# Kernel tuning notes

Measured on AMD Instinct MI355X. Metric: run time of the kernel, lower is better.

The kernel has to match this reference:

```python
import jax, jax.numpy as jnp
import numpy as np

N = 8192
F_IN = 256
F_OUT = 256


def setup_inputs() -> dict:
    key = jax.random.key(0)
    k1, k2, k3 = jax.random.split(key, 3)
    H = jax.random.normal(k1, (N, F_IN), dtype=jnp.float32)
    A_tilde = jax.random.uniform(k2, (N, N), dtype=jnp.float32)  # positive -> valid degrees
    # xavier_uniform for W: limit = sqrt(6/(fan_in+fan_out))
    limit = np.sqrt(6.0 / (F_IN + F_OUT)).astype(np.float32)
    W = jax.random.uniform(k3, (F_IN, F_OUT), dtype=jnp.float32, minval=-limit, maxval=limit)
    return {"H": H, "A_tilde": A_tilde, "W": W}


def reference(H, A_tilde, W):
    # H(l+1) = relu(D^-1/2 A D^-1/2 H W)
    # Diagonal matmuls expressed as row/col rescaling (same math, O(N^2)).
    d_inv_sqrt = jnp.sum(A_tilde, axis=1) ** -0.5          # [N]
    A_norm = d_inv_sqrt[:, None] * A_tilde * d_inv_sqrt[None, :]  # [N,N]
    H_next = (A_norm @ H) @ W                              # [N,F_out]
    return jax.nn.relu(H_next)
```

## Files before the change

### kernel.cpp

```cpp
#include <hip/hip_runtime.h>
#include <hip/hip_bf16.h>

#define N_ROWS 8192
#define F_DIM  256

typedef __bf16 bf16x8_t __attribute__((ext_vector_type(8)));
typedef float  f32x4_t  __attribute__((ext_vector_type(4)));
typedef float  f32x2_t  __attribute__((ext_vector_type(2)));

static __device__ __forceinline__ unsigned short f2bf(float x) {
    union { __hip_bfloat16 h; unsigned short u; } c;
    c.h = __float2bfloat16(x);
    return c.u;
}
static __device__ __forceinline__ unsigned pk2(float lo, float hi) {
    return (unsigned)f2bf(lo) | ((unsigned)f2bf(hi) << 16);
}

__global__ __launch_bounds__(256) void wconv_kernel(const float* __restrict__ W,
                                                    unsigned short* __restrict__ Ws) {
    const int kb = blockIdx.x;
    const int t  = threadIdx.x;
    __shared__ float wt[32][257];
    const int r = t >> 3, g = t & 7;
    const float* src = W + (kb * 32 + r) * F_DIM + g * 32;
#pragma unroll
    for (int i = 0; i < 8; ++i) {
        float4 v = *(const float4*)(src + i * 4);
        wt[r][g * 32 + i * 4 + 0] = v.x;
        wt[r][g * 32 + i * 4 + 1] = v.y;
        wt[r][g * 32 + i * 4 + 2] = v.z;
        wt[r][g * 32 + i * 4 + 3] = v.w;
    }
    __syncthreads();
    unsigned o[16];
#pragma unroll
    for (int k = 0; k < 32; k += 2) o[k >> 1] = pk2(wt[k][t], wt[k + 1][t]);
    uint4* dst = (uint4*)(Ws + kb * 8192 + t * 32);
#pragma unroll
    for (int i = 0; i < 4; ++i) dst[i] = make_uint4(o[4*i], o[4*i+1], o[4*i+2], o[4*i+3]);
}

__global__ __launch_bounds__(256) void pass1_kernel(const float* __restrict__ A,
                                                    float* __restrict__ rowsum,
                                                    unsigned short* __restrict__ As) {
    const int r    = (int)((blockIdx.x * 256 + threadIdx.x) >> 6);
    const int lane = threadIdx.x & 63;
    const float* src = A + ((size_t)r << 13) + lane * 8;
    const int m = r & 15, mt = (r >> 4) & 1;
    unsigned short* tbase = As + (size_t)(r >> 5) * (128 * 2048) + mt * 128 + m * 8;

    f32x4_t acc0 = {0.f, 0.f, 0.f, 0.f}, acc1 = {0.f, 0.f, 0.f, 0.f};
#pragma unroll 4
    for (int it = 0; it < 16; ++it) {
        const int c0 = it * 512 + lane * 8;
        f32x4_t v0 = __builtin_nontemporal_load((f32x4_t*)(src + it * 512));
        f32x4_t v1 = __builtin_nontemporal_load((f32x4_t*)(src + it * 512 + 4));
        acc0 += v0; acc1 += v1;
        uint4 pkd;
        pkd.x = pk2(v0[0], v0[1]); pkd.y = pk2(v0[2], v0[3]);
        pkd.z = pk2(v1[0], v1[1]); pkd.w = pk2(v1[2], v1[3]);
        const size_t soff = (size_t)(c0 >> 6) * 2048
                          + (size_t)((c0 >> 5) & 1) * 1024
                          + (size_t)((c0 >> 3) & 3) * 256;
        *(uint4*)(tbase + soff) = pkd;
    }
    f32x4_t a = acc0 + acc1;
    float s = (a[0] + a[1]) + (a[2] + a[3]);
#pragma unroll
    for (int off = 1; off < 64; off <<= 1) s += __shfl_xor(s, off);
    if (lane == 0) rowsum[r] = s;
}

__global__ __launch_bounds__(256) void prep2_kernel(const float* __restrict__ rowsum,
                                                    const float* __restrict__ H,
                                                    float* __restrict__ dvec,
                                                    unsigned short* __restrict__ Xs) {
    const int kb = blockIdx.x;
    const int t  = threadIdx.x;
    __shared__ float dl[32];
    __shared__ float ht[32][257];
    if (t < 32) {
        float d = 1.0f / sqrtf(rowsum[kb * 32 + t]);
        dl[t] = d;
        dvec[kb * 32 + t] = d;
    }
    __syncthreads();
    const int hr = t >> 3, hg = t & 7;
    const float* hsrc = H + (size_t)(kb * 32 + hr) * F_DIM + hg * 32;
    const float d = dl[hr];
#pragma unroll
    for (int i = 0; i < 8; ++i) {
        float4 v = *(const float4*)(hsrc + i * 4);
        ht[hr][hg * 32 + i * 4 + 0] = v.x * d;
        ht[hr][hg * 32 + i * 4 + 1] = v.y * d;
        ht[hr][hg * 32 + i * 4 + 2] = v.z * d;
        ht[hr][hg * 32 + i * 4 + 3] = v.w * d;
    }
    __syncthreads();
    unsigned o[16];
#pragma unroll
    for (int k = 0; k < 32; k += 2) o[k >> 1] = pk2(ht[k][t], ht[k + 1][t]);
    uint4* dst = (uint4*)(Xs + kb * 8192 + t * 32);
#pragma unroll
    for (int i = 0; i < 4; ++i) dst[i] = make_uint4(o[4*i], o[4*i+1], o[4*i+2], o[4*i+3]);
}

template <int KITERS>
__global__ __launch_bounds__(512) void gemm1_kernel(const unsigned short* __restrict__ As,
                                                    const unsigned short* __restrict__ Bs,
                                                    const float* __restrict__ dvec,
                                                    float* __restrict__ Y) {
    const int t    = threadIdx.x;
    const int blk  = blockIdx.x;
    const int half = blockIdx.y;
    const int w = t >> 6, l = t & 63;
    const int m = l & 15, q = l >> 4;

    const unsigned short* ap = As + ((size_t)blk * 128 + (size_t)half * KITERS) * 2048
                                  + q * 256 + m * 8;
    const unsigned short* bp = Bs + (size_t)half * KITERS * 16384 + (w * 32 + m) * 32 + q * 8;

    f32x4_t acc[2][2] = {};

    uint4 a_cur[4], b_cur[4];
    a_cur[0] = *(const uint4*)(ap);
    a_cur[1] = *(const uint4*)(ap + 128);
    a_cur[2] = *(const uint4*)(ap + 1024);
    a_cur[3] = *(const uint4*)(ap + 1152);
    b_cur[0] = *(const uint4*)(bp);
    b_cur[1] = *(const uint4*)(bp + 512);
    b_cur[2] = *(const uint4*)(bp + 8192);
    b_cur[3] = *(const uint4*)(bp + 8704);

    for (int i = 0; i < KITERS; ++i) {
        uint4 a_nxt[4], b_nxt[4];
        if (i + 1 < KITERS) {
            const unsigned short* an = ap + (size_t)(i + 1) * 2048;
            const unsigned short* bn = bp + (size_t)(i + 1) * 16384;
            a_nxt[0] = *(const uint4*)(an);
            a_nxt[1] = *(const uint4*)(an + 128);
            a_nxt[2] = *(const uint4*)(an + 1024);
            a_nxt[3] = *(const uint4*)(an + 1152);
            b_nxt[0] = *(const uint4*)(bn);
            b_nxt[1] = *(const uint4*)(bn + 512);
            b_nxt[2] = *(const uint4*)(bn + 8192);
            b_nxt[3] = *(const uint4*)(bn + 8704);
        }
#pragma unroll
        for (int s = 0; s < 2; ++s) {
            bf16x8_t af0 = __builtin_bit_cast(bf16x8_t, a_cur[s * 2 + 0]);
            bf16x8_t af1 = __builtin_bit_cast(bf16x8_t, a_cur[s * 2 + 1]);
            bf16x8_t bf0 = __builtin_bit_cast(bf16x8_t, b_cur[s * 2 + 0]);
            bf16x8_t bf1 = __builtin_bit_cast(bf16x8_t, b_cur[s * 2 + 1]);
            acc[0][0] = __builtin_amdgcn_mfma_f32_16x16x32_bf16(af0, bf0, acc[0][0], 0, 0, 0);
            acc[0][1] = __builtin_amdgcn_mfma_f32_16x16x32_bf16(af0, bf1, acc[0][1], 0, 0, 0);
            acc[1][0] = __builtin_amdgcn_mfma_f32_16x16x32_bf16(af1, bf0, acc[1][0], 0, 0, 0);
            acc[1][1] = __builtin_amdgcn_mfma_f32_16x16x32_bf16(af1, bf1, acc[1][1], 0, 0, 0);
        }
#pragma unroll
        for (int k = 0; k < 4; ++k) { a_cur[k] = a_nxt[k]; b_cur[k] = b_nxt[k]; }
    }

    float* obase = Y + (size_t)half * ((size_t)N_ROWS * F_DIM);
    const int gcol0 = w * 32 + m;
#pragma unroll
    for (int mt = 0; mt < 2; ++mt) {
#pragma unroll
        for (int r = 0; r < 4; ++r) {
            const int grow = blk * 32 + mt * 16 + q * 4 + r;
            const float ds = dvec[grow];
#pragma unroll
            for (int nt = 0; nt < 2; ++nt) {
                obase[(size_t)grow * F_DIM + gcol0 + nt * 16] = acc[mt][nt][r] * ds;
            }
        }
    }
}

template <int KITERS, int ASTRIDE>
__global__ __launch_bounds__(512) void gemm2_kernel(const float* __restrict__ Amat,
                                                    const float* __restrict__ Amat2,
                                                    const unsigned short* __restrict__ Bs,
                                                    float* __restrict__ out) {
    const int t   = threadIdx.x;
    const int blk = blockIdx.x;
    const int w = t >> 6, l = t & 63;
    const int m = l & 15, q = l >> 4;

    __shared__ __align__(16) unsigned short Al[2][1024];

    const int ar = t >> 4, ac = (t & 15) * 2;
    const float* aptr  = Amat  + (size_t)(blk * 32 + ar) * ASTRIDE + ac;
    const float* aptr2 = Amat2 + (size_t)(blk * 32 + ar) * ASTRIDE + ac;
    const int wr_idx = (ac >> 3) * 256 + (ar >> 4) * 128 + (ar & 15) * 8 + (ac & 7);

    const unsigned short* bptr = Bs + (w * 32 + m) * 32 + q * 8;

    f32x4_t acc[2][2] = {};

    f32x2_t a_cur[2]; uint4 b_cur[2][2];
#pragma unroll
    for (int s = 0; s < 2; ++s) {
        f32x2_t a1 = *(const f32x2_t*)(aptr + s * 32);
        f32x2_t a2 = *(const f32x2_t*)(aptr2 + s * 32);
        a_cur[s] = a1 + a2;
        b_cur[s][0] = *(const uint4*)(bptr + s * 8192);
        b_cur[s][1] = *(const uint4*)(bptr + s * 8192 + 512);
    }

    for (int i = 0; i < KITERS; ++i) {
        f32x2_t a_nxt[2]; uint4 b_nxt[2][2];
        if (i + 1 < KITERS) {
            const float* ap  = aptr  + (i + 1) * 64;
            const float* ap2 = aptr2 + (i + 1) * 64;
            const unsigned short* bp = bptr + (size_t)(i + 1) * 16384;
#pragma unroll
            for (int s = 0; s < 2; ++s) {
                f32x2_t a1 = *(const f32x2_t*)(ap + s * 32);
                f32x2_t a2 = *(const f32x2_t*)(ap2 + s * 32);
                a_nxt[s] = a1 + a2;
                b_nxt[s][0] = *(const uint4*)(bp + s * 8192);
                b_nxt[s][1] = *(const uint4*)(bp + s * 8192 + 512);
            }
        }
        const unsigned aw0 = pk2(a_cur[0][0], a_cur[0][1]);
        const unsigned aw1 = pk2(a_cur[1][0], a_cur[1][1]);
        __syncthreads();
        *(unsigned*)&Al[0][wr_idx] = aw0;
        *(unsigned*)&Al[1][wr_idx] = aw1;
        __syncthreads();
#pragma unroll
        for (int s = 0; s < 2; ++s) {
            bf16x8_t af0 = *(const bf16x8_t*)&Al[s][q * 256 + m * 8];
            bf16x8_t af1 = *(const bf16x8_t*)&Al[s][q * 256 + 128 + m * 8];
            bf16x8_t bf0 = __builtin_bit_cast(bf16x8_t, b_cur[s][0]);
            bf16x8_t bf1 = __builtin_bit_cast(bf16x8_t, b_cur[s][1]);
            acc[0][0] = __builtin_amdgcn_mfma_f32_16x16x32_bf16(af0, bf0, acc[0][0], 0, 0, 0);
            acc[0][1] = __builtin_amdgcn_mfma_f32_16x16x32_bf16(af0, bf1, acc[0][1], 0, 0, 0);
            acc[1][0] = __builtin_amdgcn_mfma_f32_16x16x32_bf16(af1, bf0, acc[1][0], 0, 0, 0);
            acc[1][1] = __builtin_amdgcn_mfma_f32_16x16x32_bf16(af1, bf1, acc[1][1], 0, 0, 0);
        }
#pragma unroll
        for (int s = 0; s < 2; ++s) {
            a_cur[s]    = a_nxt[s];
            b_cur[s][0] = b_nxt[s][0];
            b_cur[s][1] = b_nxt[s][1];
        }
    }

    const int gcol0 = w * 32 + m;
#pragma unroll
    for (int mt = 0; mt < 2; ++mt) {
#pragma unroll
        for (int r = 0; r < 4; ++r) {
            const int grow = blk * 32 + mt * 16 + q * 4 + r;
#pragma unroll
            for (int nt = 0; nt < 2; ++nt) {
                out[(size_t)grow * F_DIM + gcol0 + nt * 16] = fmaxf(acc[mt][nt][r], 0.f);
            }
        }
    }
}

extern "C" void kernel_launch(void* const* d_in, const int* in_sizes, int n_in,
                              void* d_out, int out_size, void* d_ws, size_t ws_size,
                              hipStream_t stream) {
    (void)in_sizes; (void)n_in; (void)out_size; (void)ws_size;
    const float* H = (const float*)d_in[0];
    const float* A = (const float*)d_in[1];
    const float* W = (const float*)d_in[2];
    float* out = (float*)d_out;

    char* ws = (char*)d_ws;
    float*          dvec   = (float*)ws;
    float*          rowsum = (float*)(ws + (32 << 10));
    unsigned short* Wsz    = (unsigned short*)(ws + (64 << 10));
    unsigned short* Xs     = (unsigned short*)(ws + (256 << 10));
    float*          Y1     = (float*)(ws + (8 << 20));
    float*          Y2     = Y1 + (size_t)N_ROWS * F_DIM;
    unsigned short* As     = (unsigned short*)(ws + (32 << 20));

    wconv_kernel<<<dim3(8),    dim3(256), 0, stream>>>(W, Wsz);
    pass1_kernel<<<dim3(2048), dim3(256), 0, stream>>>(A, rowsum, As);
    prep2_kernel<<<dim3(256),  dim3(256), 0, stream>>>(rowsum, H, dvec, Xs);
    gemm1_kernel<64><<<dim3(256, 2), dim3(512), 0, stream>>>(As, Xs, dvec, Y1);
    gemm2_kernel<4, 256><<<dim3(256), dim3(512), 0, stream>>>(Y1, Y2, Wsz, out);
}
```

Before: 515.9 us.

## Stage A bf16 conversion through swizzled LDS and share A tiles across gemm1 waves

The A-conversion pass now uses 1024-thread blocks that each handle 32 rows. Each block converts one quarter of the columns at a time into a swizzled 128KB LDS tile, then writes the packed bf16 layout to global memory with fully contiguous 16-byte stores, replacing the scattered per-row stores. gemm1 now loads each A chunk once per block into LDS, with one coalesced load per thread and prefetch of the next phase, instead of every wave reloading the same A fragments from global memory. The cost is added block-wide barriers and LDS traffic, and the 128KB LDS allocation limits occupancy.

```diff
diff --git a/kernel.cpp b/kernel.cpp
--- a/kernel.cpp
+++ b/kernel.cpp
@@ -41,35 +41,58 @@
     for (int i = 0; i < 4; ++i) dst[i] = make_uint4(o[4*i], o[4*i+1], o[4*i+2], o[4*i+3]);
 }
 
-__global__ __launch_bounds__(256) void pass1_kernel(const float* __restrict__ A,
+__global__ __launch_bounds__(1024) void prep_kernel(const float* __restrict__ A,
                                                     float* __restrict__ rowsum,
                                                     unsigned short* __restrict__ As) {
-    const int r    = (int)((blockIdx.x * 256 + threadIdx.x) >> 6);
-    const int lane = threadIdx.x & 63;
-    const float* src = A + ((size_t)r << 13) + lane * 8;
-    const int m = r & 15, mt = (r >> 4) & 1;
-    unsigned short* tbase = As + (size_t)(r >> 5) * (128 * 2048) + mt * 128 + m * 8;
-
-    f32x4_t acc0 = {0.f, 0.f, 0.f, 0.f}, acc1 = {0.f, 0.f, 0.f, 0.f};
-#pragma unroll 4
-    for (int it = 0; it < 16; ++it) {
-        const int c0 = it * 512 + lane * 8;
-        f32x4_t v0 = __builtin_nontemporal_load((f32x4_t*)(src + it * 512));
-        f32x4_t v1 = __builtin_nontemporal_load((f32x4_t*)(src + it * 512 + 4));
-        acc0 += v0; acc1 += v1;
-        uint4 pkd;
-        pkd.x = pk2(v0[0], v0[1]); pkd.y = pk2(v0[2], v0[3]);
-        pkd.z = pk2(v1[0], v1[1]); pkd.w = pk2(v1[2], v1[3]);
-        const size_t soff = (size_t)(c0 >> 6) * 2048
-                          + (size_t)((c0 >> 5) & 1) * 1024
-                          + (size_t)((c0 >> 3) & 3) * 256;
-        *(uint4*)(tbase + soff) = pkd;
-    }
-    f32x4_t a = acc0 + acc1;
-    float s = (a[0] + a[1]) + (a[2] + a[3]);
-#pragma unroll
-    for (int off = 1; off < 64; off <<= 1) s += __shfl_xor(s, off);
-    if (lane == 0) rowsum[r] = s;
+    const int kb   = blockIdx.x;
+    const int t    = threadIdx.x;
+    const int w    = t >> 6, lane = t & 63;
+    __shared__ __align__(16) char lds[131072];
+
+    const float* Ab = A + ((size_t)kb << 18);
+    f32x4_t rs0 = {0.f, 0.f, 0.f, 0.f}, rs1 = {0.f, 0.f, 0.f, 0.f};
+
+    for (int q = 0; q < 4; ++q) {
+        if (q) __syncthreads();
+#pragma unroll
+        for (int rr = 0; rr < 2; ++rr) {
+            const int r  = w * 2 + rr;
+            const int mb = (r >> 4) * 256 + (r & 15) * 16;
+            const float* rp = Ab + ((size_t)r << 13) + q * 2048;
+#pragma unroll
+            for (int ch = 0; ch < 8; ++ch) {
+                f32x4_t v = __builtin_nontemporal_load((const f32x4_t*)(rp + ch * 256 + lane * 4));
+                if (rr == 0) rs0 += v; else rs1 += v;
+                const int cq  = ch * 256 + lane * 4;
+                int byte = (cq >> 6) * 4096 + ((cq >> 5) & 1) * 2048
+                         + ((cq >> 3) & 3) * 512 + mb + ((cq & 7) ? 8 : 0);
+                byte ^= ((byte >> 9) & 7) << 4;
+                uint2 pv; pv.x = pk2(v[0], v[1]); pv.y = pk2(v[2], v[3]);
+                *(uint2*)(lds + byte) = pv;
+            }
+        }
+        __syncthreads();
+        char* dstb = (char*)As + ((size_t)(kb * 128 + q * 32)) * 4096;
+#pragma unroll
+        for (int it = 0; it < 8; ++it) {
+            const int byte = it * 16384 + t * 16;
+            const int sb   = byte ^ (((byte >> 9) & 7) << 4);
+            *(uint4*)(dstb + byte) = *(const uint4*)(lds + sb);
+        }
+    }
+    {
+        float s0 = (rs0[0] + rs0[1]) + (rs0[2] + rs0[3]);
+        float s1 = (rs1[0] + rs1[1]) + (rs1[2] + rs1[3]);
+#pragma unroll
+        for (int off = 1; off < 64; off <<= 1) {
+            s0 += __shfl_xor(s0, off);
+            s1 += __shfl_xor(s1, off);
+        }
+        if (lane == 0) {
+            rowsum[kb * 32 + w * 2 + 0] = s0;
+            rowsum[kb * 32 + w * 2 + 1] = s1;
+        }
+    }
 }
 
 __global__ __launch_bounds__(256) void prep2_kernel(const float* __restrict__ rowsum,
@@ -106,9 +129,9 @@
     for (int i = 0; i < 4; ++i) dst[i] = make_uint4(o[4*i], o[4*i+1], o[4*i+2], o[4*i+3]);
 }
 
-template <int KITERS>
+template <int PHASES>
 __global__ __launch_bounds__(512) void gemm1_kernel(const unsigned short* __restrict__ As,
-                                                    const unsigned short* __restrict__ Bs,
+                                                    const unsigned short* __restrict__ Xs,
                                                     const float* __restrict__ dvec,
                                                     float* __restrict__ Y) {
     const int t    = threadIdx.x;
@@ -117,49 +140,32 @@
     const int w = t >> 6, l = t & 63;
     const int m = l & 15, q = l >> 4;
 
-    const unsigned short* ap = As + ((size_t)blk * 128 + (size_t)half * KITERS) * 2048
-                                  + q * 256 + m * 8;
-    const unsigned short* bp = Bs + (size_t)half * KITERS * 16384 + (w * 32 + m) * 32 + q * 8;
+    __shared__ __align__(16) char lds[8192];
+
+    const char* asrc = (const char*)As + (size_t)(blk * 128 + half * 64) * 4096 + t * 16;
 
     f32x4_t acc[2][2] = {};
 
-    uint4 a_cur[4], b_cur[4];
-    a_cur[0] = *(const uint4*)(ap);
-    a_cur[1] = *(const uint4*)(ap + 128);
-    a_cur[2] = *(const uint4*)(ap + 1024);
-    a_cur[3] = *(const uint4*)(ap + 1152);
-    b_cur[0] = *(const uint4*)(bp);
-    b_cur[1] = *(const uint4*)(bp + 512);
-    b_cur[2] = *(const uint4*)(bp + 8192);
-    b_cur[3] = *(const uint4*)(bp + 8704);
-
-    for (int i = 0; i < KITERS; ++i) {
-        uint4 a_nxt[4], b_nxt[4];
-        if (i + 1 < KITERS) {
-            const unsigned short* an = ap + (size_t)(i + 1) * 2048;
-            const unsigned short* bn = bp + (size_t)(i + 1) * 16384;
-            a_nxt[0] = *(const uint4*)(an);
-            a_nxt[1] = *(const uint4*)(an + 128);
-            a_nxt[2] = *(const uint4*)(an + 1024);
-            a_nxt[3] = *(const uint4*)(an + 1152);
-            b_nxt[0] = *(const uint4*)(bn);
-            b_nxt[1] = *(const uint4*)(bn + 512);
-            b_nxt[2] = *(const uint4*)(bn + 8192);
-            b_nxt[3] = *(const uint4*)(bn + 8704);
-        }
-#pragma unroll
-        for (int s = 0; s < 2; ++s) {
-            bf16x8_t af0 = __builtin_bit_cast(bf16x8_t, a_cur[s * 2 + 0]);
-            bf16x8_t af1 = __builtin_bit_cast(bf16x8_t, a_cur[s * 2 + 1]);
-            bf16x8_t bf0 = __builtin_bit_cast(bf16x8_t, b_cur[s * 2 + 0]);
-            bf16x8_t bf1 = __builtin_bit_cast(bf16x8_t, b_cur[s * 2 + 1]);
+    uint4 apf = *(const uint4*)asrc;
+    for (int p = 0; p < PHASES; ++p) {
+        __syncthreads();
+        *(uint4*)&lds[t * 16] = apf;
+        __syncthreads();
+        if (p + 1 < PHASES) apf = *(const uint4*)(asrc + (size_t)(p + 1) * 8192);
+        const unsigned short* bp = Xs + (size_t)(half * 128 + p * 4) * 8192
+                                      + (w * 32 + m) * 32 + q * 8;
+#pragma unroll
+        for (int ss = 0; ss < 4; ++ss) {
+            const int fb = (ss >> 1) * 4096 + (ss & 1) * 2048 + q * 512 + m * 16;
+            bf16x8_t af0 = *(const bf16x8_t*)&lds[fb];
+            bf16x8_t af1 = *(const bf16x8_t*)&lds[fb + 256];
+            bf16x8_t bf0 = *(const bf16x8_t*)(bp + ss * 8192);
+            bf16x8_t bf1 = *(const bf16x8_t*)(bp + ss * 8192 + 512);
             acc[0][0] = __builtin_amdgcn_mfma_f32_16x16x32_bf16(af0, bf0, acc[0][0], 0, 0, 0);
             acc[0][1] = __builtin_amdgcn_mfma_f32_16x16x32_bf16(af0, bf1, acc[0][1], 0, 0, 0);
             acc[1][0] = __builtin_amdgcn_mfma_f32_16x16x32_bf16(af1, bf0, acc[1][0], 0, 0, 0);
             acc[1][1] = __builtin_amdgcn_mfma_f32_16x16x32_bf16(af1, bf1, acc[1][1], 0, 0, 0);
         }
-#pragma unroll
-        for (int k = 0; k < 4; ++k) { a_cur[k] = a_nxt[k]; b_cur[k] = b_nxt[k]; }
     }
 
     float* obase = Y + (size_t)half * ((size_t)N_ROWS * F_DIM);
@@ -281,9 +287,9 @@
     float*          Y2     = Y1 + (size_t)N_ROWS * F_DIM;
     unsigned short* As     = (unsigned short*)(ws + (32 << 20));
 
-    wconv_kernel<<<dim3(8),    dim3(256), 0, stream>>>(W, Wsz);
-    pass1_kernel<<<dim3(2048), dim3(256), 0, stream>>>(A, rowsum, As);
-    prep2_kernel<<<dim3(256),  dim3(256), 0, stream>>>(rowsum, H, dvec, Xs);
-    gemm1_kernel<64><<<dim3(256, 2), dim3(512), 0, stream>>>(As, Xs, dvec, Y1);
+    wconv_kernel<<<dim3(8),   dim3(256),  0, stream>>>(W, Wsz);
+    prep_kernel <<<dim3(256), dim3(1024), 0, stream>>>(A, rowsum, As);
+    prep2_kernel<<<dim3(256), dim3(256),  0, stream>>>(rowsum, H, dvec, Xs);
+    gemm1_kernel<32><<<dim3(256, 2), dim3(512), 0, stream>>>(As, Xs, dvec, Y1);
     gemm2_kernel<4, 256><<<dim3(256), dim3(512), 0, stream>>>(Y1, Y2, Wsz, out);
 }
```

After: 468.1 us. -9.3%, faster.
